# Performance work log

Measured on AMD Instinct MI355X. Metric: run time of the kernel, lower is better.

The kernel has to match this reference:

```python
import jax, jax.numpy as jnp
import numpy as np

N_NODES = 100000

def _gcn_conv(x, edge_index, W, b):
    # PyG GCNConv with normalize=False, add_self_loops=False:
    # out[dst] = sum_{(src,dst) in E} (x @ W)[src] + b
    xw = x @ W                                   # [N, out]
    src, dst = edge_index[0], edge_index[1]
    agg = jax.ops.segment_sum(xw[src], dst, num_segments=x.shape[0])  # [N, out]
    return agg + b

def setup_inputs() -> dict:
    key = jax.random.key(0)
    k1, k2, k3, k4 = jax.random.split(key, 4)
    F_in, F_hid, F_out = 128, 64, 40
    E = 1_600_000
    x = jax.random.normal(k1, (N_NODES, F_in), dtype=jnp.float32)
    edge_index = jax.random.randint(k2, (2, E), 0, N_NODES, dtype=jnp.int64)
    W1 = jax.random.normal(k3, (F_in, F_hid), dtype=jnp.float32) * (1.0 / np.sqrt(F_in))
    b1 = jnp.zeros((F_hid,), dtype=jnp.float32)
    W2 = jax.random.normal(k4, (F_hid, F_out), dtype=jnp.float32) * (1.0 / np.sqrt(F_hid))
    b2 = jnp.zeros((F_out,), dtype=jnp.float32)
    return {"x": x, "edge_index": edge_index, "W1": W1, "b1": b1, "W2": W2, "b2": b2}

def reference(x, edge_index, W1, b1, W2, b2):
    h = _gcn_conv(x, edge_index, W1, b1)
    h = jax.nn.relu(h)
    h = _gcn_conv(h, edge_index, W2, b2)
    return jax.nn.log_softmax(h, axis=1)
```

## Files before the change

### kernel.cpp

```cpp
#include <hip/hip_runtime.h>
#include <cstdint>
#include <cstddef>

#define F_IN  128
#define F_HID 64
#define F_OUT 40

#define BSH   9
#define NBMAX 256
#define CHUNK 4096

typedef __attribute__((ext_vector_type(8))) short short8;
typedef __attribute__((ext_vector_type(4))) float f32x4;

__device__ __forceinline__ unsigned short f2bf(float f) {
  unsigned u = __float_as_uint(f);
  u += 0x7fffu + ((u >> 16) & 1u);
  return (unsigned short)(u >> 16);
}
__device__ __forceinline__ float bf2f(unsigned short b) {
  return __uint_as_float((unsigned)b << 16);
}
__device__ __forceinline__ float bflo(unsigned u) { return __uint_as_float(u << 16); }
__device__ __forceinline__ float bfhi(unsigned u) { return __uint_as_float(u & 0xffff0000u); }
__device__ __forceinline__ unsigned packbf(float lo, float hi) {
  return (unsigned)f2bf(lo) | ((unsigned)f2bf(hi) << 16);
}

__global__ __launch_bounds__(256) void wcvt_k(const float* __restrict__ W1,
                                              const float* __restrict__ W2,
                                              unsigned short* __restrict__ w1s,
                                              unsigned short* __restrict__ w2s) {
  int t = threadIdx.x;
  for (int i = t; i < 8192; i += 256) {
    int f = i >> 9, r = i & 511;
    int lane = r >> 3, j = r & 7;
    int ct = f >> 2, ks = f & 3;
    int n = ct * 16 + (lane & 15);
    int k = ks * 32 + (lane >> 4) * 8 + j;
    w1s[i] = f2bf(W1[k * F_HID + n]);
  }
  for (int i = t; i < 3072; i += 256) {
    int f = i >> 9, r = i & 511;
    int lane = r >> 3, j = r & 7;
    int ct = f >> 1, ks = f & 1;
    int n = ct * 16 + (lane & 15);
    int k = ks * 32 + (lane >> 4) * 8 + j;
    w2s[i] = (n < F_OUT) ? f2bf(W2[k * F_OUT + n]) : (unsigned short)0;
  }
}

__global__ __launch_bounds__(256) void front_k(const float* __restrict__ x,
                                               const float* __restrict__ W1,
                                               const unsigned short* __restrict__ w1s,
                                               unsigned short* __restrict__ xw, int N,
                                               const int* __restrict__ ei,
                                               int* __restrict__ counts,
                                               int E, int NBLK, int NBUCK) {
  __shared__ int lh[NBMAX];
  if ((int)blockIdx.x < NBLK) {
    int t = threadIdx.x, blk = blockIdx.x;
    lh[t] = 0;
    __syncthreads();
    int e0 = blk * CHUNK;
    int n = min(CHUNK, E - e0);
    for (int i = t; i < n; i += 256)
      atomicAdd(&lh[((unsigned)ei[E + e0 + i]) >> BSH], 1);
    __syncthreads();
    if (t < NBUCK) counts[t * NBLK + blk] = lh[t];
    return;
  }
  int gblk = blockIdx.x - NBLK;
  int lane = threadIdx.x & 63;
  int wid  = gblk * 4 + (threadIdx.x >> 6);
  int row0 = wid * 16;
  if (row0 >= N) return;
  int m = lane & 15, q = lane >> 4;

  if (row0 + 16 <= N) {
    short8 b[16];
#pragma unroll
    for (int f = 0; f < 16; ++f)
      b[f] = *(const short8*)(w1s + f * 512 + lane * 8);

    short8 a[4];
#pragma unroll
    for (int ks = 0; ks < 4; ++ks) {
      const float* xp = x + (size_t)(row0 + m) * F_IN + ks * 32 + q * 8;
      float4 v0 = *(const float4*)xp;
      float4 v1 = *(const float4*)(xp + 4);
      short8 t;
      t[0] = (short)f2bf(v0.x); t[1] = (short)f2bf(v0.y);
      t[2] = (short)f2bf(v0.z); t[3] = (short)f2bf(v0.w);
      t[4] = (short)f2bf(v1.x); t[5] = (short)f2bf(v1.y);
      t[6] = (short)f2bf(v1.z); t[7] = (short)f2bf(v1.w);
      a[ks] = t;
    }

    f32x4 z = {0.f, 0.f, 0.f, 0.f};
    f32x4 acc[4] = {z, z, z, z};
#pragma unroll
    for (int ct = 0; ct < 4; ++ct)
#pragma unroll
      for (int ks = 0; ks < 4; ++ks)
        acc[ct] = __builtin_amdgcn_mfma_f32_16x16x32_bf16(a[ks], b[ct * 4 + ks],
                                                          acc[ct], 0, 0, 0);
#pragma unroll
    for (int ct = 0; ct < 4; ++ct)
#pragma unroll
      for (int r = 0; r < 4; ++r) {
        int row = row0 + q * 4 + r;
        xw[(size_t)row * F_HID + ct * 16 + m] = f2bf(acc[ct][r]);
      }
  } else {
    for (int r = 0; r < 16 && row0 + r < N; ++r) {
      const float* xr = x + (size_t)(row0 + r) * F_IN;
      float s = 0.f;
      for (int k = 0; k < F_IN; ++k) s = fmaf(xr[k], W1[k * F_HID + lane], s);
      xw[(size_t)(row0 + r) * F_HID + lane] = f2bf(s);
    }
  }
}

__global__ __launch_bounds__(256) void scanA_k(const int* __restrict__ a,
                                               int* __restrict__ psum, int M) {
  int t = threadIdx.x;
  int base = blockIdx.x * 2048 + t * 8;
  int s = 0;
#pragma unroll
  for (int j = 0; j < 8; ++j) if (base + j < M) s += a[base + j];
#pragma unroll
  for (int off = 32; off; off >>= 1) s += __shfl_xor(s, off, 64);
  __shared__ int sm[4];
  if ((t & 63) == 0) sm[t >> 6] = s;
  __syncthreads();
  if (t == 0) psum[blockIdx.x] = sm[0] + sm[1] + sm[2] + sm[3];
}

__global__ __launch_bounds__(256) void scanB_k(int* __restrict__ psum, int nb) {
  __shared__ int sm[256];
  int t = threadIdx.x;
  int v = (t < nb) ? psum[t] : 0;
  sm[t] = v;
  __syncthreads();
  for (int off = 1; off < 256; off <<= 1) {
    int add = (t >= off) ? sm[t - off] : 0;
    __syncthreads();
    sm[t] += add;
    __syncthreads();
  }
  if (t < nb) psum[t] = sm[t] - v;
}

__global__ __launch_bounds__(256) void scanC_k(int* __restrict__ a,
                                               const int* __restrict__ psum,
                                               int M, int E) {
  __shared__ int sm[256];
  int t = threadIdx.x;
  int base = blockIdx.x * 2048 + t * 8;
  int v[8];
  int s = 0;
#pragma unroll
  for (int j = 0; j < 8; ++j) {
    v[j] = (base + j < M) ? a[base + j] : 0;
    s += v[j];
  }
  sm[t] = s;
  __syncthreads();
  for (int off = 1; off < 256; off <<= 1) {
    int add = (t >= off) ? sm[t - off] : 0;
    __syncthreads();
    sm[t] += add;
    __syncthreads();
  }
  int run = psum[blockIdx.x] + sm[t] - s;
#pragma unroll
  for (int j = 0; j < 8; ++j) {
    if (base + j < M) a[base + j] = run;
    run += v[j];
  }
  if (blockIdx.x == 0 && t == 0) a[M] = E;
}

__global__ __launch_bounds__(256) void partition_k(const int* __restrict__ bases,
                                                   const int* __restrict__ ei,
                                                   uint2* __restrict__ ebuf,
                                                   int E, int NBLK, int NBUCK) {
  __shared__ uint2 slots[CHUNK];
  __shared__ int scn[NBMAX], lcur[NBMAX], gadj[NBMAX];
  int t = threadIdx.x, blk = blockIdx.x;
  int e0 = blk * CHUNK;
  int n = min(CHUNK, E - e0);

  int i0 = t * NBLK + blk;
  int cnt = 0, base0 = 0;
  if (t < NBUCK) {
    base0 = bases[i0];
    cnt = bases[i0 + 1] - base0;
  }
  scn[t] = cnt;
  __syncthreads();
  for (int off = 1; off < 256; off <<= 1) {
    int add = (t >= off) ? scn[t - off] : 0;
    __syncthreads();
    scn[t] += add;
    __syncthreads();
  }
  int excl = scn[t] - cnt;
  if (t < NBUCK) { lcur[t] = excl; gadj[t] = base0 - excl; }
  __syncthreads();

  for (int i = t; i < n; i += 256) {
    int s = ei[e0 + i], d = ei[E + e0 + i];
    int pos = atomicAdd(&lcur[((unsigned)d) >> BSH], 1);
    slots[pos] = make_uint2((unsigned)s, (unsigned)d);
  }
  __syncthreads();
  for (int i = t; i < n; i += 256) {
    uint2 sd = slots[i];
    ebuf[gadj[sd.y >> BSH] + i] = sd;
  }
}

__global__ __launch_bounds__(256) void build_k(const uint2* __restrict__ ebuf,
                                               const int* __restrict__ bases,
                                               int* __restrict__ row_ptr,
                                               int* __restrict__ csr,
                                               int N, int E, int NBLK, int NBUCK) {
  __shared__ int hist[512];
  __shared__ int psc[256];
  int t = threadIdx.x, b = blockIdx.x;
  int nodeBase = b << BSH;
  int S = bases[b * NBLK];
  int T = bases[(b + 1) * NBLK];

  hist[t] = 0; hist[t + 256] = 0;
  __syncthreads();
  for (int i = S + t; i < T; i += 256)
    atomicAdd(&hist[ebuf[i].y & 511u], 1);
  __syncthreads();

  int v0 = hist[2 * t], v1 = hist[2 * t + 1];
  int pair = v0 + v1;
  psc[t] = pair;
  __syncthreads();
  for (int off = 1; off < 256; off <<= 1) {
    int add = (t >= off) ? psc[t - off] : 0;
    __syncthreads();
    psc[t] += add;
    __syncthreads();
  }
  int ep = psc[t] - pair;
  int e0 = ep, e1 = ep + v0;

  int node0 = nodeBase + 2 * t;
  if (node0 < N) row_ptr[node0] = S + e0;
  if (node0 + 1 < N) row_ptr[node0 + 1] = S + e1;
  if (b == 0 && t == 0) row_ptr[N] = E;

  hist[2 * t] = e0; hist[2 * t + 1] = e1;
  __syncthreads();
  for (int i = S + t; i < T; i += 256) {
    uint2 sd = ebuf[i];
    int pos = atomicAdd(&hist[sd.y & 511u], 1);
    csr[S + pos] = (int)sd.x;
  }
}

__global__ __launch_bounds__(256) void agg1_k(const unsigned short* __restrict__ xw,
                                              const int* __restrict__ row_ptr,
                                              const int* __restrict__ csr,
                                              const float* __restrict__ b1,
                                              unsigned short* __restrict__ h, int N) {
  int row = (blockIdx.x * 256 + threadIdx.x) >> 6;
  int lane = threadIdx.x & 63;
  if (row >= N) return;
  int slot = lane >> 3, part = lane & 7;
  int start = row_ptr[row], end = row_ptr[row + 1];

  float acc[8], bcc[8];
#pragma unroll
  for (int j = 0; j < 8; ++j) { acc[j] = 0.f; bcc[j] = 0.f; }

  for (int base = start; base < end; base += 16) {
    int i0 = base + slot, i1 = base + 8 + slot;
    if (i0 < end) {
      int s = csr[i0];
      uint4 v = *(const uint4*)(xw + ((size_t)s << 6) + (part << 3));
      acc[0] += bflo(v.x); acc[1] += bfhi(v.x);
      acc[2] += bflo(v.y); acc[3] += bfhi(v.y);
      acc[4] += bflo(v.z); acc[5] += bfhi(v.z);
      acc[6] += bflo(v.w); acc[7] += bfhi(v.w);
    }
    if (i1 < end) {
      int s = csr[i1];
      uint4 v = *(const uint4*)(xw + ((size_t)s << 6) + (part << 3));
      bcc[0] += bflo(v.x); bcc[1] += bfhi(v.x);
      bcc[2] += bflo(v.y); bcc[3] += bfhi(v.y);
      bcc[4] += bflo(v.z); bcc[5] += bfhi(v.z);
      bcc[6] += bflo(v.w); bcc[7] += bfhi(v.w);
    }
  }
#pragma unroll
  for (int j = 0; j < 8; ++j) acc[j] += bcc[j];
#pragma unroll
  for (int off = 8; off < 64; off <<= 1) {
#pragma unroll
    for (int j = 0; j < 8; ++j) acc[j] += __shfl_xor(acc[j], off, 64);
  }
  if (slot == 0) {
    int c0 = part << 3;
    float4 bA = *(const float4*)(b1 + c0);
    float4 bB = *(const float4*)(b1 + c0 + 4);
    float r0 = fmaxf(acc[0] + bA.x, 0.f), r1 = fmaxf(acc[1] + bA.y, 0.f);
    float r2 = fmaxf(acc[2] + bA.z, 0.f), r3 = fmaxf(acc[3] + bA.w, 0.f);
    float r4 = fmaxf(acc[4] + bB.x, 0.f), r5 = fmaxf(acc[5] + bB.y, 0.f);
    float r6 = fmaxf(acc[6] + bB.z, 0.f), r7 = fmaxf(acc[7] + bB.w, 0.f);
    uint4 o = make_uint4(packbf(r0, r1), packbf(r2, r3), packbf(r4, r5), packbf(r6, r7));
    *(uint4*)(h + ((size_t)row << 6) + c0) = o;
  }
}

__global__ __launch_bounds__(256) void gemm2_k(const unsigned short* __restrict__ h,
                                               const float* __restrict__ W2,
                                               const unsigned short* __restrict__ w2s,
                                               unsigned short* __restrict__ hw, int N) {
  int lane = threadIdx.x & 63;
  int wid  = (blockIdx.x * 256 + threadIdx.x) >> 6;
  int row0 = wid * 16;
  if (row0 >= N) return;
  int m = lane & 15, q = lane >> 4;

  if (row0 + 16 <= N) {
    short8 b[6];
#pragma unroll
    for (int f = 0; f < 6; ++f)
      b[f] = *(const short8*)(w2s + f * 512 + lane * 8);

    short8 a[2];
#pragma unroll
    for (int ks = 0; ks < 2; ++ks)
      a[ks] = *(const short8*)(h + (size_t)(row0 + m) * F_HID + ks * 32 + q * 8);

    f32x4 z = {0.f, 0.f, 0.f, 0.f};
    f32x4 acc[3] = {z, z, z};
#pragma unroll
    for (int ct = 0; ct < 3; ++ct)
#pragma unroll
      for (int ks = 0; ks < 2; ++ks)
        acc[ct] = __builtin_amdgcn_mfma_f32_16x16x32_bf16(a[ks], b[ct * 2 + ks],
                                                          acc[ct], 0, 0, 0);
#pragma unroll
    for (int ct = 0; ct < 3; ++ct)
#pragma unroll
      for (int r = 0; r < 4; ++r) {
        int row = row0 + q * 4 + r;
        int c = ct * 16 + m;
        hw[(size_t)row * F_HID + c] = (c < F_OUT) ? f2bf(acc[ct][r]) : (unsigned short)0;
      }
#pragma unroll
    for (int r = 0; r < 4; ++r) {
      int row = row0 + q * 4 + r;
      hw[(size_t)row * F_HID + 48 + m] = 0;
    }
  } else {
    for (int r = 0; r < 16 && row0 + r < N; ++r) {
      const unsigned short* hr = h + (size_t)(row0 + r) * F_HID;
      float s = 0.f;
      if (lane < F_OUT)
        for (int k = 0; k < F_HID; ++k) s = fmaf(bf2f(hr[k]), W2[k * F_OUT + lane], s);
      hw[(size_t)(row0 + r) * F_HID + lane] =
          (lane < F_OUT) ? f2bf(s) : (unsigned short)0;
    }
  }
}

__global__ __launch_bounds__(256) void agg2_ls_k(const unsigned short* __restrict__ hw,
                                                 const int* __restrict__ row_ptr,
                                                 const int* __restrict__ csr,
                                                 const float* __restrict__ b2,
                                                 float* __restrict__ out, int N) {
  int row = (blockIdx.x * 256 + threadIdx.x) >> 6;
  int lane = threadIdx.x & 63;
  if (row >= N) return;
  int slot = lane >> 3, part = lane & 7;
  int start = row_ptr[row], end = row_ptr[row + 1];

  float acc[8], bcc[8];
#pragma unroll
  for (int j = 0; j < 8; ++j) { acc[j] = 0.f; bcc[j] = 0.f; }

  for (int base = start; base < end; base += 16) {
    int i0 = base + slot, i1 = base + 8 + slot;
    if (i0 < end) {
      int s = csr[i0];
      uint4 v = *(const uint4*)(hw + ((size_t)s << 6) + (part << 3));
      acc[0] += bflo(v.x); acc[1] += bfhi(v.x);
      acc[2] += bflo(v.y); acc[3] += bfhi(v.y);
      acc[4] += bflo(v.z); acc[5] += bfhi(v.z);
      acc[6] += bflo(v.w); acc[7] += bfhi(v.w);
    }
    if (i1 < end) {
      int s = csr[i1];
      uint4 v = *(const uint4*)(hw + ((size_t)s << 6) + (part << 3));
      bcc[0] += bflo(v.x); bcc[1] += bfhi(v.x);
      bcc[2] += bflo(v.y); bcc[3] += bfhi(v.y);
      bcc[4] += bflo(v.z); bcc[5] += bfhi(v.z);
      bcc[6] += bflo(v.w); bcc[7] += bfhi(v.w);
    }
  }
#pragma unroll
  for (int j = 0; j < 8; ++j) acc[j] += bcc[j];
#pragma unroll
  for (int off = 8; off < 64; off <<= 1) {
#pragma unroll
    for (int j = 0; j < 8; ++j) acc[j] += __shfl_xor(acc[j], off, 64);
  }

  float vj[8];
  float m = -3.4e38f;
  if (part < 5) {
    int c0 = part << 3;
    float4 bA = *(const float4*)(b2 + c0);
    float4 bB = *(const float4*)(b2 + c0 + 4);
    vj[0] = acc[0] + bA.x; vj[1] = acc[1] + bA.y;
    vj[2] = acc[2] + bA.z; vj[3] = acc[3] + bA.w;
    vj[4] = acc[4] + bB.x; vj[5] = acc[5] + bB.y;
    vj[6] = acc[6] + bB.z; vj[7] = acc[7] + bB.w;
#pragma unroll
    for (int j = 0; j < 8; ++j) m = fmaxf(m, vj[j]);
  }
#pragma unroll
  for (int off = 1; off < 8; off <<= 1) m = fmaxf(m, __shfl_xor(m, off, 64));
  float ex = 0.f;
  if (part < 5) {
#pragma unroll
    for (int j = 0; j < 8; ++j) ex += __expf(vj[j] - m);
  }
#pragma unroll
  for (int off = 1; off < 8; off <<= 1) ex += __shfl_xor(ex, off, 64);
  float lse = __logf(ex) + m;

  if (slot == 0 && part < 5) {
    int c0 = part << 3;
    float* op = out + (size_t)row * F_OUT + c0;
    *(float4*)op = make_float4(vj[0] - lse, vj[1] - lse, vj[2] - lse, vj[3] - lse);
    *(float4*)(op + 4) = make_float4(vj[4] - lse, vj[5] - lse, vj[6] - lse, vj[7] - lse);
  }
}

extern "C" void kernel_launch(void* const* d_in, const int* in_sizes, int n_in,
                              void* d_out, int out_size, void* d_ws, size_t ws_size,
                              hipStream_t stream) {
  const float* x  = (const float*)d_in[0];
  const int*   ei = (const int*)d_in[1];
  const float* W1 = (const float*)d_in[2];
  const float* b1 = (const float*)d_in[3];
  const float* W2 = (const float*)d_in[4];
  const float* b2 = (const float*)d_in[5];

  int N = in_sizes[0] / F_IN;
  int E = in_sizes[1] / 2;

  char* base = (char*)d_ws;
  size_t szA = (size_t)N * F_HID * sizeof(unsigned short);
  size_t szB = (size_t)E * sizeof(uint2);
  if (szA > szB) szB = szA;
  unsigned short* xw = (unsigned short*)base;
  char* regB = base + ((szA + 255) & ~(size_t)255);
  unsigned short* h  = (unsigned short*)regB;
  uint2* ebuf        = (uint2*)regB;
  int* row_ptr = (int*)(regB + ((szB + 255) & ~(size_t)255));
  int* csr     = row_ptr + N + 1;
  int* counts  = csr + E;
  unsigned short* hw = xw;
  float* out = (float*)d_out;

  int rowsGrid = (N * 64 + 255) / 256;
  int gemmGrid = (N + 63) / 64;
  int NBLK  = (E + CHUNK - 1) / CHUNK;
  int NBUCK = (N + 511) >> BSH;
  int M = NBUCK * NBLK;
  int* psum = counts + M + 1;
  unsigned short* w1s = (unsigned short*)(psum + 64);
  unsigned short* w2s = w1s + 8192;
  int scanBlocks = (M + 2047) / 2048;

  wcvt_k<<<1, 256, 0, stream>>>(W1, W2, w1s, w2s);

  front_k<<<NBLK + gemmGrid, 256, 0, stream>>>(x, W1, w1s, xw, N,
                                               ei, counts, E, NBLK, NBUCK);

  scanA_k<<<scanBlocks, 256, 0, stream>>>(counts, psum, M);
  scanB_k<<<1, 256, 0, stream>>>(psum, scanBlocks);
  scanC_k<<<scanBlocks, 256, 0, stream>>>(counts, psum, M, E);
  partition_k<<<NBLK, 256, 0, stream>>>(counts, ei, ebuf, E, NBLK, NBUCK);
  build_k<<<NBUCK, 256, 0, stream>>>(ebuf, counts, row_ptr, csr, N, E, NBLK, NBUCK);

  agg1_k<<<rowsGrid, 256, 0, stream>>>(xw, row_ptr, csr, b1, h, N);
  gemm2_k<<<gemmGrid, 256, 0, stream>>>(h, W2, w2s, hw, N);
  agg2_ls_k<<<rowsGrid, 256, 0, stream>>>(hw, row_ptr, csr, b2, out, N);
}
```

Before: 264.7 us.

## Assign eight rows per wavefront in aggregation kernels, dropping cross-slot shuffle reductions

Both aggregation kernels now map each 8-lane group to its own destination row, so one wavefront handles 8 rows instead of 1 and the grid shrinks eightfold. Each group walks its row's edges sequentially, two at a time, which removes the 24 cross-lane shuffle-add reductions per row and the mostly idle lanes on low-degree rows. In exchange, per-lane serial work grows with row degree, there is divergence across rows of different degree within a wave, and fewer independent loads are in flight per row.

```diff
diff --git a/kernel.cpp b/kernel.cpp
--- a/kernel.cpp
+++ b/kernel.cpp
@@ -272,50 +272,57 @@
                                               const int* __restrict__ csr,
                                               const float* __restrict__ b1,
                                               unsigned short* __restrict__ h, int N) {
-  int row = (blockIdx.x * 256 + threadIdx.x) >> 6;
+  int wid = (blockIdx.x * 256 + threadIdx.x) >> 6;
   int lane = threadIdx.x & 63;
-  if (row >= N) return;
-  int slot = lane >> 3, part = lane & 7;
-  int start = row_ptr[row], end = row_ptr[row + 1];
+  int rowBase = wid * 8;
+  if (rowBase >= N) return;
+  int row = rowBase + (lane >> 3);
+  int part = lane & 7;
+  bool live = row < N;
+
+  int start = live ? row_ptr[row] : 0;
+  int end   = live ? row_ptr[row + 1] : 0;
 
   float acc[8], bcc[8];
 #pragma unroll
   for (int j = 0; j < 8; ++j) { acc[j] = 0.f; bcc[j] = 0.f; }
 
-  for (int base = start; base < end; base += 16) {
-    int i0 = base + slot, i1 = base + 8 + slot;
-    if (i0 < end) {
-      int s = csr[i0];
-      uint4 v = *(const uint4*)(xw + ((size_t)s << 6) + (part << 3));
-      acc[0] += bflo(v.x); acc[1] += bfhi(v.x);
-      acc[2] += bflo(v.y); acc[3] += bfhi(v.y);
-      acc[4] += bflo(v.z); acc[5] += bfhi(v.z);
-      acc[6] += bflo(v.w); acc[7] += bfhi(v.w);
-    }
-    if (i1 < end) {
-      int s = csr[i1];
-      uint4 v = *(const uint4*)(xw + ((size_t)s << 6) + (part << 3));
-      bcc[0] += bflo(v.x); bcc[1] += bfhi(v.x);
-      bcc[2] += bflo(v.y); bcc[3] += bfhi(v.y);
-      bcc[4] += bflo(v.z); bcc[5] += bfhi(v.z);
-      bcc[6] += bflo(v.w); bcc[7] += bfhi(v.w);
-    }
-  }
-#pragma unroll
-  for (int j = 0; j < 8; ++j) acc[j] += bcc[j];
-#pragma unroll
-  for (int off = 8; off < 64; off <<= 1) {
-#pragma unroll
-    for (int j = 0; j < 8; ++j) acc[j] += __shfl_xor(acc[j], off, 64);
-  }
-  if (slot == 0) {
+  int i = start;
+  for (; i + 1 < end; i += 2) {
+    int s0 = csr[i];
+    int s1 = csr[i + 1];
+    uint4 v0 = *(const uint4*)(xw + ((size_t)s0 << 6) + (part << 3));
+    uint4 v1 = *(const uint4*)(xw + ((size_t)s1 << 6) + (part << 3));
+    acc[0] += bflo(v0.x); acc[1] += bfhi(v0.x);
+    acc[2] += bflo(v0.y); acc[3] += bfhi(v0.y);
+    acc[4] += bflo(v0.z); acc[5] += bfhi(v0.z);
+    acc[6] += bflo(v0.w); acc[7] += bfhi(v0.w);
+    bcc[0] += bflo(v1.x); bcc[1] += bfhi(v1.x);
+    bcc[2] += bflo(v1.y); bcc[3] += bfhi(v1.y);
+    bcc[4] += bflo(v1.z); bcc[5] += bfhi(v1.z);
+    bcc[6] += bflo(v1.w); bcc[7] += bfhi(v1.w);
+  }
+  if (i < end) {
+    int s = csr[i];
+    uint4 v = *(const uint4*)(xw + ((size_t)s << 6) + (part << 3));
+    acc[0] += bflo(v.x); acc[1] += bfhi(v.x);
+    acc[2] += bflo(v.y); acc[3] += bfhi(v.y);
+    acc[4] += bflo(v.z); acc[5] += bfhi(v.z);
+    acc[6] += bflo(v.w); acc[7] += bfhi(v.w);
+  }
+
+  if (live) {
     int c0 = part << 3;
     float4 bA = *(const float4*)(b1 + c0);
     float4 bB = *(const float4*)(b1 + c0 + 4);
-    float r0 = fmaxf(acc[0] + bA.x, 0.f), r1 = fmaxf(acc[1] + bA.y, 0.f);
-    float r2 = fmaxf(acc[2] + bA.z, 0.f), r3 = fmaxf(acc[3] + bA.w, 0.f);
-    float r4 = fmaxf(acc[4] + bB.x, 0.f), r5 = fmaxf(acc[5] + bB.y, 0.f);
-    float r6 = fmaxf(acc[6] + bB.z, 0.f), r7 = fmaxf(acc[7] + bB.w, 0.f);
+    float r0 = fmaxf(acc[0] + bcc[0] + bA.x, 0.f);
+    float r1 = fmaxf(acc[1] + bcc[1] + bA.y, 0.f);
+    float r2 = fmaxf(acc[2] + bcc[2] + bA.z, 0.f);
+    float r3 = fmaxf(acc[3] + bcc[3] + bA.w, 0.f);
+    float r4 = fmaxf(acc[4] + bcc[4] + bB.x, 0.f);
+    float r5 = fmaxf(acc[5] + bcc[5] + bB.y, 0.f);
+    float r6 = fmaxf(acc[6] + bcc[6] + bB.z, 0.f);
+    float r7 = fmaxf(acc[7] + bcc[7] + bB.w, 0.f);
     uint4 o = make_uint4(packbf(r0, r1), packbf(r2, r3), packbf(r4, r5), packbf(r6, r7));
     *(uint4*)(h + ((size_t)row << 6) + c0) = o;
   }
@@ -380,60 +387,63 @@
                                                  const int* __restrict__ csr,
                                                  const float* __restrict__ b2,
                                                  float* __restrict__ out, int N) {
-  int row = (blockIdx.x * 256 + threadIdx.x) >> 6;
+  int wid = (blockIdx.x * 256 + threadIdx.x) >> 6;
   int lane = threadIdx.x & 63;
-  if (row >= N) return;
-  int slot = lane >> 3, part = lane & 7;
-  int start = row_ptr[row], end = row_ptr[row + 1];
+  int rowBase = wid * 8;
+  if (rowBase >= N) return;
+  int row = rowBase + (lane >> 3);
+  int part = lane & 7;
+  bool live = row < N;
+
+  int start = live ? row_ptr[row] : 0;
+  int end   = live ? row_ptr[row + 1] : 0;
 
   float acc[8], bcc[8];
 #pragma unroll
   for (int j = 0; j < 8; ++j) { acc[j] = 0.f; bcc[j] = 0.f; }
 
-  for (int base = start; base < end; base += 16) {
-    int i0 = base + slot, i1 = base + 8 + slot;
-    if (i0 < end) {
-      int s = csr[i0];
-      uint4 v = *(const uint4*)(hw + ((size_t)s << 6) + (part << 3));
-      acc[0] += bflo(v.x); acc[1] += bfhi(v.x);
-      acc[2] += bflo(v.y); acc[3] += bfhi(v.y);
-      acc[4] += bflo(v.z); acc[5] += bfhi(v.z);
-      acc[6] += bflo(v.w); acc[7] += bfhi(v.w);
-    }
-    if (i1 < end) {
-      int s = csr[i1];
-      uint4 v = *(const uint4*)(hw + ((size_t)s << 6) + (part << 3));
-      bcc[0] += bflo(v.x); bcc[1] += bfhi(v.x);
-      bcc[2] += bflo(v.y); bcc[3] += bfhi(v.y);
-      bcc[4] += bflo(v.z); bcc[5] += bfhi(v.z);
-      bcc[6] += bflo(v.w); bcc[7] += bfhi(v.w);
-    }
-  }
-#pragma unroll
-  for (int j = 0; j < 8; ++j) acc[j] += bcc[j];
-#pragma unroll
-  for (int off = 8; off < 64; off <<= 1) {
-#pragma unroll
-    for (int j = 0; j < 8; ++j) acc[j] += __shfl_xor(acc[j], off, 64);
-  }
-
+  int i = start;
+  for (; i + 1 < end; i += 2) {
+    int s0 = csr[i];
+    int s1 = csr[i + 1];
+    uint4 v0 = *(const uint4*)(hw + ((size_t)s0 << 6) + (part << 3));
+    uint4 v1 = *(const uint4*)(hw + ((size_t)s1 << 6) + (part << 3));
+    acc[0] += bflo(v0.x); acc[1] += bfhi(v0.x);
+    acc[2] += bflo(v0.y); acc[3] += bfhi(v0.y);
+    acc[4] += bflo(v0.z); acc[5] += bfhi(v0.z);
+    acc[6] += bflo(v0.w); acc[7] += bfhi(v0.w);
+    bcc[0] += bflo(v1.x); bcc[1] += bfhi(v1.x);
+    bcc[2] += bflo(v1.y); bcc[3] += bfhi(v1.y);
+    bcc[4] += bflo(v1.z); bcc[5] += bfhi(v1.z);
+    bcc[6] += bflo(v1.w); bcc[7] += bfhi(v1.w);
+  }
+  if (i < end) {
+    int s = csr[i];
+    uint4 v = *(const uint4*)(hw + ((size_t)s << 6) + (part << 3));
+    acc[0] += bflo(v.x); acc[1] += bfhi(v.x);
+    acc[2] += bflo(v.y); acc[3] += bfhi(v.y);
+    acc[4] += bflo(v.z); acc[5] += bfhi(v.z);
+    acc[6] += bflo(v.w); acc[7] += bfhi(v.w);
+  }
+
+  bool valid = live && (part < 5);
   float vj[8];
   float m = -3.4e38f;
-  if (part < 5) {
+  if (valid) {
     int c0 = part << 3;
     float4 bA = *(const float4*)(b2 + c0);
     float4 bB = *(const float4*)(b2 + c0 + 4);
-    vj[0] = acc[0] + bA.x; vj[1] = acc[1] + bA.y;
-    vj[2] = acc[2] + bA.z; vj[3] = acc[3] + bA.w;
-    vj[4] = acc[4] + bB.x; vj[5] = acc[5] + bB.y;
-    vj[6] = acc[6] + bB.z; vj[7] = acc[7] + bB.w;
+    vj[0] = acc[0] + bcc[0] + bA.x; vj[1] = acc[1] + bcc[1] + bA.y;
+    vj[2] = acc[2] + bcc[2] + bA.z; vj[3] = acc[3] + bcc[3] + bA.w;
+    vj[4] = acc[4] + bcc[4] + bB.x; vj[5] = acc[5] + bcc[5] + bB.y;
+    vj[6] = acc[6] + bcc[6] + bB.z; vj[7] = acc[7] + bcc[7] + bB.w;
 #pragma unroll
     for (int j = 0; j < 8; ++j) m = fmaxf(m, vj[j]);
   }
 #pragma unroll
   for (int off = 1; off < 8; off <<= 1) m = fmaxf(m, __shfl_xor(m, off, 64));
   float ex = 0.f;
-  if (part < 5) {
+  if (valid) {
 #pragma unroll
     for (int j = 0; j < 8; ++j) ex += __expf(vj[j] - m);
   }
@@ -441,7 +451,7 @@
   for (int off = 1; off < 8; off <<= 1) ex += __shfl_xor(ex, off, 64);
   float lse = __logf(ex) + m;
 
-  if (slot == 0 && part < 5) {
+  if (valid) {
     int c0 = part << 3;
     float* op = out + (size_t)row * F_OUT + c0;
     *(float4*)op = make_float4(vj[0] - lse, vj[1] - lse, vj[2] - lse, vj[3] - lse);
@@ -476,7 +486,7 @@
   unsigned short* hw = xw;
   float* out = (float*)d_out;
 
-  int rowsGrid = (N * 64 + 255) / 256;
+  int aggGrid  = (N * 8 + 255) / 256;
   int gemmGrid = (N + 63) / 64;
   int NBLK  = (E + CHUNK - 1) / CHUNK;
   int NBUCK = (N + 511) >> BSH;
@@ -497,7 +507,7 @@
   partition_k<<<NBLK, 256, 0, stream>>>(counts, ei, ebuf, E, NBLK, NBUCK);
   build_k<<<NBUCK, 256, 0, stream>>>(ebuf, counts, row_ptr, csr, N, E, NBLK, NBUCK);
 
-  agg1_k<<<rowsGrid, 256, 0, stream>>>(xw, row_ptr, csr, b1, h, N);
+  agg1_k<<<aggGrid, 256, 0, stream>>>(xw, row_ptr, csr, b1, h, N);
   gemm2_k<<<gemmGrid, 256, 0, stream>>>(h, W2, w2s, hw, N);
-  agg2_ls_k<<<rowsGrid, 256, 0, stream>>>(hw, row_ptr, csr, b2, out, N);
-}
+  agg2_ls_k<<<aggGrid, 256, 0, stream>>>(hw, row_ptr, csr, b2, out, N);
+}
```

Result: faster. 236.3 us (-10.7%).
